# Optimization experiments

Measured on AMD Instinct MI355X. Metric: run time of the kernel, lower is better.

Reference implementation:

```python
import jax, jax.numpy as jnp
import numpy as np

N_NODES = 100000
N_EDGES = 3200000
N_FEAT = 128
HIDDEN = 16
N_CLASSES = 10
N_GRAPHS = 512


def setup_inputs() -> dict:
    key = jax.random.key(0)
    ks = jax.random.split(key, 12)
    x = jax.random.normal(ks[0], (N_NODES, N_FEAT), dtype=jnp.float32)
    edge_index = jax.random.randint(ks[1], (2, N_EDGES), 0, N_NODES, dtype=jnp.int64)
    batch = jnp.sort(jax.random.randint(ks[2], (N_NODES,), 0, N_GRAPHS, dtype=jnp.int64))
    def glorot(k, fan_in, fan_out):
        s = jnp.sqrt(6.0 / (fan_in + fan_out)).astype(jnp.float32)
        return jax.random.uniform(k, (fan_in, fan_out), jnp.float32, -s, s)
    W1 = glorot(ks[3], N_FEAT, HIDDEN); b1 = jnp.zeros((HIDDEN,), jnp.float32)
    W2 = glorot(ks[4], HIDDEN, HIDDEN); b2 = jnp.zeros((HIDDEN,), jnp.float32)
    W3 = glorot(ks[5], HIDDEN, HIDDEN); b3 = jnp.zeros((HIDDEN,), jnp.float32)
    Wlin = glorot(ks[6], HIDDEN, N_CLASSES)
    blin = jnp.zeros((N_CLASSES,), jnp.float32)
    return {"x": x, "edge_index": edge_index, "batch": batch,
            "W1": W1, "b1": b1, "W2": W2, "b2": b2, "W3": W3, "b3": b3,
            "Wlin": Wlin, "blin": blin}


def _gcn_conv(x, W, b, src, dst, norm, n):
    # h = X W ; out[dst] += norm * h[src] ; + bias
    h = x @ W
    out = jax.ops.segment_sum(h[src] * norm[:, None], dst, num_segments=n)
    return out + b


def reference(x, edge_index, batch, W1, b1, W2, b2, W3, b3, Wlin, blin):
    n = x.shape[0]
    loop = jnp.arange(n, dtype=edge_index.dtype)
    src = jnp.concatenate([edge_index[0], loop])  # add self-loops (PyG GCNConv default)
    dst = jnp.concatenate([edge_index[1], loop])
    # symmetric degree normalization: deg over destination (incl. self-loops)
    deg = jax.ops.segment_sum(jnp.ones_like(dst, dtype=x.dtype), dst, num_segments=n)
    dinv = jnp.where(deg > 0, jax.lax.rsqrt(jnp.maximum(deg, 1.0)), 0.0)
    norm = dinv[src] * dinv[dst]  # [E+N]

    h = jax.nn.relu(_gcn_conv(x, W1, b1, src, dst, norm, n))
    h = jax.nn.relu(_gcn_conv(h, W2, b2, src, dst, norm, n))
    h = _gcn_conv(h, W3, b3, src, dst, norm, n)
    # global add pool over graphs
    pooled = jax.ops.segment_sum(h, batch, num_segments=N_GRAPHS)  # [G, hidden]
    # dropout p=0.5 is identity in eval mode
    return pooled @ Wlin + blin
```

## Files before the change

### kernel.cpp

```cpp
#include <hip/hip_runtime.h>
#include <hip/hip_fp16.h>

#define N_NODES   100000
#define N_EDGES   3200000
#define N_FEAT    128
#define HIDDEN    16
#define N_CLASSES 10
#define N_GRAPHS  512
#define NPB       256
#define NBUCKET   391
#define EPB       4096
#define PBLK      ((N_EDGES + EPB - 1) / EPB)
#define PSLACK    15872
#define CSLACK    9216


__global__ void cursor_init_kernel(int* __restrict__ cur) {
    int i = blockIdx.x * 256 + threadIdx.x;
    if (i < NBUCKET) cur[i] = i * PSLACK;
}

__global__ __launch_bounds__(512) void partition_kernel(const int* __restrict__ src,
                                                        const int* __restrict__ dst,
                                                        int* __restrict__ cur,
                                                        unsigned* __restrict__ part) {
    __shared__ int cnt[NBUCKET];
    __shared__ int lbase[NBUCKET];
    __shared__ int rk[NBUCKET];
    __shared__ int gbase[NBUCKET];
    __shared__ int s[512];
    __shared__ unsigned sorted[EPB];
    __shared__ unsigned short bb[EPB];
    __shared__ unsigned char  dl[EPB];
    int tid = threadIdx.x;
    for (int i = tid; i < NBUCKET; i += 512) cnt[i] = 0;
    __syncthreads();
    int s0 = blockIdx.x * EPB;
#pragma unroll
    for (int i = 0; i < EPB / 512; ++i) {
        int le = i * 512 + tid;
        int e  = s0 + le;
        if (e < N_EDGES) {
            int d = dst[e];
            int b = d >> 8;
            bb[le] = (unsigned short)b;
            dl[le] = (unsigned char)(d & 255);
            atomicAdd(&cnt[b], 1);
        }
    }
    __syncthreads();
    int v = (tid < NBUCKET) ? cnt[tid] : 0;
    s[tid] = v;
    __syncthreads();
    for (int off = 1; off < 512; off <<= 1) {
        int t = (tid >= off) ? s[tid - off] : 0;
        __syncthreads();
        s[tid] += t;
        __syncthreads();
    }
    if (tid < NBUCKET) {
        int lb = s[tid] - v;
        lbase[tid] = lb;
        rk[tid]    = lb;
        int cpad = (v + 15) & ~15;
        gbase[tid] = cpad ? atomicAdd(&cur[tid], cpad) : 0;
    }
    __syncthreads();
#pragma unroll
    for (int i = 0; i < EPB / 512; ++i) {
        int le = i * 512 + tid;
        int e  = s0 + le;
        if (e < N_EDGES) {
            int b = bb[le];
            int r = atomicAdd(&rk[b], 1);
            sorted[r] = (unsigned)src[e] | ((unsigned)dl[le] << 17);
        }
    }
    __syncthreads();
    int w16 = tid >> 4, l16 = tid & 15;
    for (int b = w16; b < NBUCKET; b += 32) {
        int c = cnt[b];
        if (!c) continue;
        int cpad = (c + 15) & ~15;
        int lb = lbase[b], gb = gbase[b];
        for (int j = l16; j < cpad; j += 16)
            part[gb + j] = (j < c) ? sorted[lb + j] : 0xFFFFFFFFu;
    }
}

__global__ __launch_bounds__(512) void build_csr_kernel(const unsigned* __restrict__ part,
                                                        const int* __restrict__ cur,
                                                        int2* __restrict__ rp,
                                                        float* __restrict__ dinv, int* __restrict__ csr) {
    __shared__ int ncnt[256];
    __shared__ int s[512];
    int b   = blockIdx.x;
    int tid = threadIdx.x;
    int beg = b * PSLACK, end = cur[b];
    if (tid < 256) ncnt[tid] = 0;
    __syncthreads();
    for (int j = beg + tid; j < end; j += 512) {
        unsigned r = part[j];
        if (r != 0xFFFFFFFFu) atomicAdd(&ncnt[(r >> 17) & 255], 1);
    }
    __syncthreads();
    int deg = (tid < 256) ? ncnt[tid] : 0;
    s[tid] = deg;
    __syncthreads();
    for (int off = 1; off < 512; off <<= 1) {
        int t = (tid >= off) ? s[tid - off] : 0;
        __syncthreads();
        s[tid] += t;
        __syncthreads();
    }
    int excl = s[tid] - deg;
    int cbeg = b * CSLACK;
    if (tid < 256) {
        int node = b * 256 + tid;
        if (node < N_NODES) {
            rp[node]   = make_int2(cbeg + excl, cbeg + excl + deg);
            dinv[node] = rsqrtf((float)(deg + 1));
        }
    }
    __syncthreads();
    if (tid < 256) ncnt[tid] = cbeg + excl;
    __syncthreads();
    for (int j = beg + tid; j < end; j += 512) {
        unsigned r = part[j];
        if (r != 0xFFFFFFFFu) {
            int vv = (r >> 17) & 255;
            int slot = atomicAdd(&ncnt[vv], 1);
            csr[slot] = (int)(r & 0x1FFFFu);
        }
    }
}


__device__ __forceinline__ void pack_store8(__half* outp, int idx, const float* o) {
    int4 w;
    __half2 q;
    q = __floats2half2_rn(o[0], o[1]); w.x = *(int*)&q;
    q = __floats2half2_rn(o[2], o[3]); w.y = *(int*)&q;
    q = __floats2half2_rn(o[4], o[5]); w.z = *(int*)&q;
    q = __floats2half2_rn(o[6], o[7]); w.w = *(int*)&q;
    ((int4*)outp)[idx] = w;
}

__global__ void transform_x_kernel(const float* __restrict__ x, const float* __restrict__ W,
                                   const float* __restrict__ dinv, __half* __restrict__ g) {
    __shared__ float Wl[N_FEAT * HIDDEN];
    int tid = threadIdx.x;
    for (int i = tid; i < N_FEAT * HIDDEN; i += 256) Wl[i] = W[i];
    __syncthreads();
    int v = blockIdx.x * 256 + tid;
    if (v >= N_NODES) return;
    float acc[HIDDEN];
#pragma unroll
    for (int f = 0; f < HIDDEN; ++f) acc[f] = 0.f;
    const float4* xr = (const float4*)(x + (size_t)v * N_FEAT);
#pragma unroll 4
    for (int k4 = 0; k4 < N_FEAT / 4; ++k4) {
        float4 xv = xr[k4];
        const float* wr = &Wl[k4 * 4 * HIDDEN];
#pragma unroll
        for (int f = 0; f < HIDDEN; ++f)
            acc[f] += xv.x * wr[f] + xv.y * wr[HIDDEN + f] +
                      xv.z * wr[2 * HIDDEN + f] + xv.w * wr[3 * HIDDEN + f];
    }
    float di = dinv[v];
#pragma unroll
    for (int f = 0; f < HIDDEN; ++f) acc[f] *= di;
    pack_store8(g, v * 2,     &acc[0]);
    pack_store8(g, v * 2 + 1, &acc[8]);
}

template <int MODE>
__global__ __launch_bounds__(256) void aggregate_kernel(
        const __half* __restrict__ g, const int2* __restrict__ rp,
        const int* __restrict__ csr, const float* __restrict__ dinv,
        const float* __restrict__ bias, const float* __restrict__ Wn,
        __half* __restrict__ out) {
    __shared__ float WnL[HIDDEN * HIDDEN];
    int tid  = threadIdx.x;
    if (MODE == 2) {
        if (tid < HIDDEN * HIDDEN) WnL[tid] = Wn[tid];
        __syncthreads();
    }
    int wave = tid >> 6;
    int l    = tid & 63;
    int c  = l >> 3;
    int vl = (l >> 1) & 3;
    int hh = l & 1;
    int v = blockIdx.x * 16 + wave * 4 + vl;
    int2 range = rp[v];
    int beg = range.x, end = range.y;
    const int4* g4 = (const int4*)g;
    float a0 = 0.f, a1 = 0.f, a2 = 0.f, a3 = 0.f, a4 = 0.f, a5 = 0.f, a6 = 0.f, a7 = 0.f;
#pragma unroll 4
    for (int j = beg + c; j < end; j += 8) {
        int s = csr[j];
        int4 r = g4[s * 2 + hh];
        float2 f0 = __half22float2(*(const __half2*)&r.x);
        float2 f1 = __half22float2(*(const __half2*)&r.y);
        float2 f2 = __half22float2(*(const __half2*)&r.z);
        float2 f3 = __half22float2(*(const __half2*)&r.w);
        a0 += f0.x; a1 += f0.y; a2 += f1.x; a3 += f1.y;
        a4 += f2.x; a5 += f2.y; a6 += f3.x; a7 += f3.y;
    }
    a0 += __shfl_xor(a0, 8);  a1 += __shfl_xor(a1, 8);
    a2 += __shfl_xor(a2, 8);  a3 += __shfl_xor(a3, 8);
    a4 += __shfl_xor(a4, 8);  a5 += __shfl_xor(a5, 8);
    a6 += __shfl_xor(a6, 8);  a7 += __shfl_xor(a7, 8);
    a0 += __shfl_xor(a0, 16); a1 += __shfl_xor(a1, 16);
    a2 += __shfl_xor(a2, 16); a3 += __shfl_xor(a3, 16);
    a4 += __shfl_xor(a4, 16); a5 += __shfl_xor(a5, 16);
    a6 += __shfl_xor(a6, 16); a7 += __shfl_xor(a7, 16);
    a0 += __shfl_xor(a0, 32); a1 += __shfl_xor(a1, 32);
    a2 += __shfl_xor(a2, 32); a3 += __shfl_xor(a3, 32);
    a4 += __shfl_xor(a4, 32); a5 += __shfl_xor(a5, 32);
    a6 += __shfl_xor(a6, 32); a7 += __shfl_xor(a7, 32);
    if (c == 0) {
        int4 r = g4[v * 2 + hh];
        float2 s0 = __half22float2(*(const __half2*)&r.x);
        float2 s1 = __half22float2(*(const __half2*)&r.y);
        float2 s2 = __half22float2(*(const __half2*)&r.z);
        float2 s3 = __half22float2(*(const __half2*)&r.w);
        float di = dinv[v];
        const float4* bp = (const float4*)bias;
        float4 bA = bp[hh * 2];
        float4 bB = bp[hh * 2 + 1];
        float o[8];
        o[0] = di * (a0 + s0.x) + bA.x;
        o[1] = di * (a1 + s0.y) + bA.y;
        o[2] = di * (a2 + s1.x) + bA.z;
        o[3] = di * (a3 + s1.y) + bA.w;
        o[4] = di * (a4 + s2.x) + bB.x;
        o[5] = di * (a5 + s2.y) + bB.y;
        o[6] = di * (a6 + s3.x) + bB.z;
        o[7] = di * (a7 + s3.y) + bB.w;
        if (MODE == 2) {
#pragma unroll
            for (int i = 0; i < 8; ++i) o[i] = fmaxf(o[i], 0.f);
            float pa[16];
#pragma unroll
            for (int f = 0; f < 16; ++f) pa[f] = 0.f;
            const float* wr = &WnL[hh * 8 * HIDDEN];
#pragma unroll
            for (int q = 0; q < 8; ++q) {
                float hq = o[q];
#pragma unroll
                for (int f = 0; f < 16; ++f) pa[f] += hq * wr[q * HIDDEN + f];
            }
            float o2[8];
#pragma unroll
            for (int i = 0; i < 8; ++i) {
                float lo = pa[i];
                float hi = pa[8 + i];
                float keep = hh ? hi : lo;
                float send = hh ? lo : hi;
                float recv = __shfl_xor(send, 1);
                o2[i] = di * (keep + recv);
            }
            pack_store8(out, v * 2 + hh, o2);
        } else {
            pack_store8(out, v * 2 + hh, o);
        }
    }
}


__global__ void pool_head_kernel(const __half* __restrict__ h, const int* __restrict__ batch,
                                 const float* __restrict__ Wlin, const float* __restrict__ blin,
                                 float* __restrict__ out) {
    __shared__ float red[256];
    __shared__ int bounds[2];
    int g   = blockIdx.x;
    int tid = threadIdx.x;
    if (tid < 2) {
        int target = g + tid;
        int lo = 0, hi = N_NODES;
        while (lo < hi) {
            int mid = (lo + hi) >> 1;
            if (batch[mid] < target) lo = mid + 1; else hi = mid;
        }
        bounds[tid] = lo;
    }
    __syncthreads();
    int start = bounds[0], end = bounds[1];
    int f = tid & 15, r = tid >> 4;
    float acc = 0.f;
    for (int v = start + r; v < end; v += 16)
        acc += __half2float(h[v * HIDDEN + f]);
    red[tid] = acc;
    __syncthreads();
    for (int off = 128; off >= 16; off >>= 1) {
        if (tid < off) red[tid] += red[tid + off];
        __syncthreads();
    }
    if (tid < N_CLASSES) {
        float s = blin[tid];
#pragma unroll
        for (int fe = 0; fe < HIDDEN; ++fe) s += red[fe] * Wlin[fe * N_CLASSES + tid];
        out[g * N_CLASSES + tid] = s;
    }
}


extern "C" void kernel_launch(void* const* d_in, const int* in_sizes, int n_in,
                              void* d_out, int out_size, void* d_ws, size_t ws_size,
                              hipStream_t stream) {
    const float* x     = (const float*)d_in[0];
    const int*   ei    = (const int*)d_in[1];
    const int*   src   = ei;
    const int*   dst   = ei + N_EDGES;
    const int*   batch = (const int*)d_in[2];
    const float* W1 = (const float*)d_in[3];
    const float* b1 = (const float*)d_in[4];
    const float* W2 = (const float*)d_in[5];
    const float* b2 = (const float*)d_in[6];
    const float* W3 = (const float*)d_in[7];
    const float* b3 = (const float*)d_in[8];
    const float* Wlin = (const float*)d_in[9];
    const float* blin = (const float*)d_in[10];
    float* out = (float*)d_out;

    char* w = (char*)d_ws;
    auto alloc = [&](size_t bytes) -> char* {
        char* p = w;
        w += (bytes + 255) & ~(size_t)255;
        return p;
    };
    int*    cur    = (int*)alloc((size_t)NBUCKET * 4);
    int2*   rp     = (int2*)alloc((size_t)N_NODES * 8);
    float*  dinv   = (float*)alloc((size_t)N_NODES * 4);
    __half* gA     = (__half*)alloc((size_t)N_NODES * HIDDEN * 2);
    __half* gB     = (__half*)alloc((size_t)N_NODES * HIDDEN * 2);
    __half* hA     = (__half*)alloc((size_t)N_NODES * HIDDEN * 2);
    unsigned* part = (unsigned*)alloc((size_t)NBUCKET * PSLACK * 4);
    int*    csr    = (int*)alloc((size_t)NBUCKET * CSLACK * 4);

    int nbn = (N_NODES + 255) / 256;
    int ab  = (N_NODES + 15) / 16;

    cursor_init_kernel<<<(NBUCKET + 255) / 256, 256, 0, stream>>>(cur);
    partition_kernel<<<PBLK, 512, 0, stream>>>(src, dst, cur, part);
    build_csr_kernel<<<NBUCKET, 512, 0, stream>>>(part, cur, rp, dinv, csr);

    transform_x_kernel<<<nbn, 256, 0, stream>>>(x, W1, dinv, gA);
    aggregate_kernel<2><<<ab, 256, 0, stream>>>(gA, rp, csr, dinv, b1, W2, gB);
    aggregate_kernel<2><<<ab, 256, 0, stream>>>(gB, rp, csr, dinv, b2, W3, gA);
    aggregate_kernel<0><<<ab, 256, 0, stream>>>(gA, rp, csr, dinv, b3, nullptr, hA);

    pool_head_kernel<<<N_GRAPHS, 256, 0, stream>>>(hA, batch, Wlin, blin, out);
}
```

Baseline: 270.5 us.

## Rework partition/CSR ranking, split transform across lane pairs, prefetch aggregate gathers

Result: slower. 299.1 us (+10.6%).

```diff
diff --git a/kernel.cpp b/kernel.cpp
--- a/kernel.cpp
+++ b/kernel.cpp
@@ -26,12 +26,11 @@
                                                         unsigned* __restrict__ part) {
     __shared__ int cnt[NBUCKET];
     __shared__ int lbase[NBUCKET];
-    __shared__ int rk[NBUCKET];
     __shared__ int gbase[NBUCKET];
     __shared__ int s[512];
+    __shared__ unsigned val[EPB];
+    __shared__ unsigned br[EPB];
     __shared__ unsigned sorted[EPB];
-    __shared__ unsigned short bb[EPB];
-    __shared__ unsigned char  dl[EPB];
     int tid = threadIdx.x;
     for (int i = tid; i < NBUCKET; i += 512) cnt[i] = 0;
     __syncthreads();
@@ -41,11 +40,14 @@
         int le = i * 512 + tid;
         int e  = s0 + le;
         if (e < N_EDGES) {
-            int d = dst[e];
-            int b = d >> 8;
-            bb[le] = (unsigned short)b;
-            dl[le] = (unsigned char)(d & 255);
-            atomicAdd(&cnt[b], 1);
+            int d  = dst[e];
+            int sv = src[e];
+            int b  = d >> 8;
+            int r  = atomicAdd(&cnt[b], 1);
+            val[le] = (unsigned)sv | ((unsigned)(d & 255) << 17);
+            br[le]  = (unsigned)b | ((unsigned)r << 16);
+        } else {
+            br[le] = 0xFFFFFFFFu;
         }
     }
     __syncthreads();
@@ -59,21 +61,19 @@
         __syncthreads();
     }
     if (tid < NBUCKET) {
-        int lb = s[tid] - v;
-        lbase[tid] = lb;
-        rk[tid]    = lb;
+        lbase[tid] = s[tid] - v;
         int cpad = (v + 15) & ~15;
-        gbase[tid] = cpad ? atomicAdd(&cur[tid], cpad) : 0;
+        gbase[tid] = tid * PSLACK + (cpad ? atomicAdd(&cur[tid], cpad) - tid * PSLACK : 0);
     }
     __syncthreads();
 #pragma unroll
     for (int i = 0; i < EPB / 512; ++i) {
         int le = i * 512 + tid;
-        int e  = s0 + le;
-        if (e < N_EDGES) {
-            int b = bb[le];
-            int r = atomicAdd(&rk[b], 1);
-            sorted[r] = (unsigned)src[e] | ((unsigned)dl[le] << 17);
+        unsigned w = br[le];
+        if (w != 0xFFFFFFFFu) {
+            int b = (int)(w & 0xFFFFu);
+            int r = (int)(w >> 16);
+            sorted[lbase[b] + r] = val[le];
         }
     }
     __syncthreads();
@@ -94,6 +94,7 @@
                                                         float* __restrict__ dinv, int* __restrict__ csr) {
     __shared__ int ncnt[256];
     __shared__ int s[512];
+    __shared__ unsigned char rkb[PSLACK];
     int b   = blockIdx.x;
     int tid = threadIdx.x;
     int beg = b * PSLACK, end = cur[b];
@@ -101,7 +102,8 @@
     __syncthreads();
     for (int j = beg + tid; j < end; j += 512) {
         unsigned r = part[j];
-        if (r != 0xFFFFFFFFu) atomicAdd(&ncnt[(r >> 17) & 255], 1);
+        if (r != 0xFFFFFFFFu)
+            rkb[j - beg] = (unsigned char)atomicAdd(&ncnt[(r >> 17) & 255], 1);
     }
     __syncthreads();
     int deg = (tid < 256) ? ncnt[tid] : 0;
@@ -127,11 +129,8 @@
     __syncthreads();
     for (int j = beg + tid; j < end; j += 512) {
         unsigned r = part[j];
-        if (r != 0xFFFFFFFFu) {
-            int vv = (r >> 17) & 255;
-            int slot = atomicAdd(&ncnt[vv], 1);
-            csr[slot] = (int)(r & 0x1FFFFu);
-        }
+        if (r != 0xFFFFFFFFu)
+            csr[ncnt[(r >> 17) & 255] + rkb[j - beg]] = (int)(r & 0x1FFFFu);
     }
 }
 
@@ -152,26 +151,29 @@
     int tid = threadIdx.x;
     for (int i = tid; i < N_FEAT * HIDDEN; i += 256) Wl[i] = W[i];
     __syncthreads();
-    int v = blockIdx.x * 256 + tid;
+    int t = blockIdx.x * 256 + tid;
+    int v = t >> 1;
+    int p = t & 1;
     if (v >= N_NODES) return;
     float acc[HIDDEN];
 #pragma unroll
     for (int f = 0; f < HIDDEN; ++f) acc[f] = 0.f;
-    const float4* xr = (const float4*)(x + (size_t)v * N_FEAT);
+    const float4* xr = (const float4*)(x + (size_t)v * N_FEAT + p * 64);
 #pragma unroll 4
-    for (int k4 = 0; k4 < N_FEAT / 4; ++k4) {
+    for (int k4 = 0; k4 < 16; ++k4) {
         float4 xv = xr[k4];
-        const float* wr = &Wl[k4 * 4 * HIDDEN];
+        const float* wr = &Wl[(p * 64 + k4 * 4) * HIDDEN];
 #pragma unroll
         for (int f = 0; f < HIDDEN; ++f)
             acc[f] += xv.x * wr[f] + xv.y * wr[HIDDEN + f] +
                       xv.z * wr[2 * HIDDEN + f] + xv.w * wr[3 * HIDDEN + f];
     }
+#pragma unroll
+    for (int f = 0; f < HIDDEN; ++f) acc[f] += __shfl_xor(acc[f], 1);
     float di = dinv[v];
 #pragma unroll
     for (int f = 0; f < HIDDEN; ++f) acc[f] *= di;
-    pack_store8(g, v * 2,     &acc[0]);
-    pack_store8(g, v * 2 + 1, &acc[8]);
+    pack_store8(g, v * 2 + p, &acc[p * 8]);
 }
 
 template <int MODE>
@@ -196,14 +198,21 @@
     int beg = range.x, end = range.y;
     const int4* g4 = (const int4*)g;
     float a0 = 0.f, a1 = 0.f, a2 = 0.f, a3 = 0.f, a4 = 0.f, a5 = 0.f, a6 = 0.f, a7 = 0.f;
-#pragma unroll 4
-    for (int j = beg + c; j < end; j += 8) {
-        int s = csr[j];
-        int4 r = g4[s * 2 + hh];
-        float2 f0 = __half22float2(*(const __half2*)&r.x);
-        float2 f1 = __half22float2(*(const __half2*)&r.y);
-        float2 f2 = __half22float2(*(const __half2*)&r.z);
-        float2 f3 = __half22float2(*(const __half2*)&r.w);
+    int j0 = beg + c;
+    int s_nxt = 0;
+    int4 r_cur = make_int4(0, 0, 0, 0);
+    if (j0 < end)     r_cur = g4[(size_t)csr[j0] * 2 + hh];
+    if (j0 + 8 < end) s_nxt = csr[j0 + 8];
+#pragma unroll 1
+    for (int j = j0; j < end; j += 8) {
+        int s_pf = s_nxt;
+        if (j + 16 < end) s_nxt = csr[j + 16];
+        int4 r_use = r_cur;
+        if (j + 8 < end) r_cur = g4[s_pf * 2 + hh];
+        float2 f0 = __half22float2(*(const __half2*)&r_use.x);
+        float2 f1 = __half22float2(*(const __half2*)&r_use.y);
+        float2 f2 = __half22float2(*(const __half2*)&r_use.z);
+        float2 f3 = __half22float2(*(const __half2*)&r_use.w);
         a0 += f0.x; a1 += f0.y; a2 += f1.x; a3 += f1.y;
         a4 += f2.x; a5 += f2.y; a6 += f3.x; a7 += f3.y;
     }
@@ -339,14 +348,14 @@
     unsigned* part = (unsigned*)alloc((size_t)NBUCKET * PSLACK * 4);
     int*    csr    = (int*)alloc((size_t)NBUCKET * CSLACK * 4);
 
-    int nbn = (N_NODES + 255) / 256;
+    int ntx = (2 * N_NODES + 255) / 256;
     int ab  = (N_NODES + 15) / 16;
 
     cursor_init_kernel<<<(NBUCKET + 255) / 256, 256, 0, stream>>>(cur);
     partition_kernel<<<PBLK, 512, 0, stream>>>(src, dst, cur, part);
     build_csr_kernel<<<NBUCKET, 512, 0, stream>>>(part, cur, rp, dinv, csr);
 
-    transform_x_kernel<<<nbn, 256, 0, stream>>>(x, W1, dinv, gA);
+    transform_x_kernel<<<ntx, 256, 0, stream>>>(x, W1, dinv, gA);
     aggregate_kernel<2><<<ab, 256, 0, stream>>>(gA, rp, csr, dinv, b1, W2, gB);
     aggregate_kernel<2><<<ab, 256, 0, stream>>>(gB, rp, csr, dinv, b2, W3, gA);
     aggregate_kernel<0><<<ab, 256, 0, stream>>>(gA, rp, csr, dinv, b3, nullptr, hA);
```
